# Performance work log

Measured on AMD Instinct MI355X. Metric: run time of the kernel, lower is better.

## Reference

```python
import math
import jax, jax.numpy as jnp
import numpy as np

B, T, F = 2, 1024, 1024
H, DK, DV = 16, 64, 64
OUT = 1024


def _rel_shift_left(x):
    # x: (b, h, t1, t2); Transformer-XL left shift + tril mask (causal part)
    b, h, t1, t2 = x.shape
    xp = jnp.pad(x, ((0, 0), (0, 0), (0, 0), (1, 0)))
    xp = xp.reshape(b, h, t2 + 1, t1)[:, :, 1:].reshape(b, h, t1, t2)
    tril = jnp.tril(jnp.ones((t1, t2), x.dtype), t2 - t1)
    return xp * tril


def _rel_shift_right(x):
    # x: (b, h, t1, t2); right shift + triu mask (non-causal part)
    b, h, t1, t2 = x.shape
    xp = jnp.pad(x, ((0, 0), (0, 0), (0, 0), (0, 1)))
    xp = xp.reshape(b, h, t2 + 1, t1)[:, :, :-1].reshape(b, h, t1, t2)
    triu = jnp.triu(jnp.ones((t1, t2), x.dtype), t2 - t1 + 1)
    return xp * triu


def setup_inputs() -> dict:
    key = jax.random.key(0)
    ks = jax.random.split(key, 16)
    s = 0.02
    return {
        'query': jax.random.normal(ks[0], (B, T, F), jnp.float32),
        'key': jax.random.normal(ks[1], (B, T, F), jnp.float32),
        'value': jax.random.normal(ks[2], (B, T, F), jnp.float32),
        'pos_emb': jax.random.normal(ks[3], (1, T, F), jnp.float32),
        'Wq': jax.random.normal(ks[4], (H * DK, F), jnp.float32) * s,
        'bq': jnp.zeros((H * DK,), jnp.float32),
        'Wk': jax.random.normal(ks[5], (H * DK, F), jnp.float32) * s,
        'bk': jnp.zeros((H * DK,), jnp.float32),
        'Wv': jax.random.normal(ks[6], (H * DV, F), jnp.float32) * s,
        'bv': jnp.zeros((H * DV,), jnp.float32),
        'Wp': jax.random.normal(ks[7], (H * DK, F), jnp.float32) * s,
        'bp': jnp.zeros((H * DK,), jnp.float32),
        'Wo': jax.random.normal(ks[8], (OUT, H * DV), jnp.float32) * s,
        'bo': jnp.zeros((OUT,), jnp.float32),
        'u_bias': jax.random.normal(ks[9], (H, DK), jnp.float32) * s,
        'v_bias': jax.random.normal(ks[10], (H, DK), jnp.float32) * s,
    }


def reference(query, key, value, pos_emb, Wq, bq, Wk, bk, Wv, bv, Wp, bp, Wo, bo, u_bias, v_bias):
    b, t1, _ = query.shape
    t2 = key.shape[1]
    q = (query @ Wq.T + bq).reshape(b, t1, H, DK)          # (b, t1, h, dk)
    k = (key @ Wk.T + bk).reshape(b, t2, H, DK).transpose(0, 2, 1, 3)   # (b, h, t2, dk)
    v = (value @ Wv.T + bv).reshape(b, t2, H, DV).transpose(0, 2, 1, 3) # (b, h, t2, dv)
    p = (pos_emb @ Wp.T + bp).reshape(pos_emb.shape[0], -1, H, DK).transpose(0, 2, 1, 3)[0]  # (h, t2, dk)

    q_plus_u = (q + u_bias).transpose(0, 2, 1, 3)  # (b, h, t1, dk)
    q_plus_v = (q + v_bias).transpose(0, 2, 1, 3)  # (b, h, t1, dk)

    AC = jnp.einsum('bhtd,bhsd->bhts', q_plus_u, k)
    BD = _rel_shift_left(jnp.einsum('bhtd,hsd->bhts', q_plus_v, p))
    # non-causal part: flip pos embeddings along time, right shift
    BD = BD + _rel_shift_right(jnp.einsum('bhtd,hsd->bhts', q_plus_v, jnp.flip(p, axis=1)))

    scores = (AC + BD) / math.sqrt(DK)
    attn = jax.nn.softmax(scores, axis=-1)
    x = jnp.einsum('bhts,bhsd->bthd', attn, v).reshape(b, t1, H * DV)
    return x @ Wo.T + bo
```

## Files before the change

kernel.cpp:

```cpp
#include <hip/hip_runtime.h>
#include <hip/hip_bf16.h>
#include <stdint.h>

typedef __attribute__((ext_vector_type(8))) short bf16x8;
typedef __attribute__((ext_vector_type(4))) float f32x4;
typedef __attribute__((ext_vector_type(4))) short short4v;
typedef __attribute__((ext_vector_type(2))) unsigned u32x2;

#define SCALE2 0.18033688011112042f

__device__ __forceinline__ short f2b(float f) {
  union { float f; unsigned u; } un; un.f = f;
  unsigned r = un.u + 0x7FFFu + ((un.u >> 16) & 1u);
  return (short)(r >> 16);
}

#define GLDS(GP, LP) __builtin_amdgcn_global_load_lds( \
    (__attribute__((address_space(1))) void*)(GP), \
    (__attribute__((address_space(3))) void*)(LP), 16, 0, 0)

struct CvtTab { const float* s[12]; short* d[12]; };

__global__ void cvt_all(CvtTab tab) {
  int chunk = blockIdx.x >> 10;
  int off = (blockIdx.x & 1023) * 256 + threadIdx.x;
  float4 v = *((const float4*)tab.s[chunk] + off);
  short4v o;
  o[0] = f2b(v.x); o[1] = f2b(v.y); o[2] = f2b(v.z); o[3] = f2b(v.w);
  *((short4v*)tab.d[chunk] + off) = o;
}

__device__ __forceinline__ void gemm_core128(
    const short* __restrict__ A, const short* __restrict__ W,
    int tile_m, int tile_n, short* lds, f32x4 acc[4][4])
{
  const int tid = threadIdx.x;
  const int wave = tid >> 6, lane = tid & 63;
  const int wr = wave >> 1, wc = wave & 1;
  const int q15 = lane & 15, q4 = lane >> 4;
  const int rl = lane >> 3;
  const int cswz = ((lane & 7) * 16) ^ (rl << 4);

#pragma unroll
  for (int i = 0; i < 4; ++i)
#pragma unroll
    for (int j = 0; j < 4; ++j) acc[i][j] = (f32x4){0.f, 0.f, 0.f, 0.f};

  auto stage = [&](int buf, int k0) {
    short* As = lds + buf * 16384;
    short* Bs = As + 8192;
#pragma unroll
    for (int s = 0; s < 4; ++s) {
      int ia = wave * 4 + s;
      int row = ia * 8 + rl;
      GLDS(A + (size_t)(tile_m + row) * 1024 + k0 + (cswz >> 1), (char*)As + ia * 1024);
      GLDS(W + (size_t)(tile_n + row) * 1024 + k0 + (cswz >> 1), (char*)Bs + ia * 1024);
    }
  };

  stage(0, 0);
  __syncthreads();
  for (int t = 0; t < 16; ++t) {
    const int cur = t & 1;
    if (t < 15) stage(cur ^ 1, (t + 1) * 64);
    const short* As = lds + cur * 16384;
    const short* Bs = As + 8192;
#pragma unroll
    for (int kk = 0; kk < 2; ++kk) {
      const int kbyte = kk * 64 + q4 * 16;
      const int rswz = (q15 & 7) << 4;
      bf16x8 af[4], bfr[4];
#pragma unroll
      for (int i = 0; i < 4; ++i)
        af[i] = *(const bf16x8*)((const char*)As + (wr * 64 + i * 16 + q15) * 128 + (kbyte ^ rswz));
#pragma unroll
      for (int j = 0; j < 4; ++j)
        bfr[j] = *(const bf16x8*)((const char*)Bs + (wc * 64 + j * 16 + q15) * 128 + (kbyte ^ rswz));
#pragma unroll
      for (int i = 0; i < 4; ++i)
#pragma unroll
        for (int j = 0; j < 4; ++j)
          acc[i][j] = __builtin_amdgcn_mfma_f32_16x16x32_bf16(af[i], bfr[j], acc[i][j], 0, 0, 0);
    }
    __syncthreads();
  }
}

__global__ __launch_bounds__(256)
void gemm_qkvp(const short* __restrict__ q_in, const short* __restrict__ k_in,
               const short* __restrict__ v_in, const short* __restrict__ p_in,
               const short* __restrict__ wq, const short* __restrict__ wk,
               const short* __restrict__ wv, const short* __restrict__ wp,
               const float* __restrict__ bq, const float* __restrict__ bk,
               const float* __restrict__ bv, const float* __restrict__ bp,
               const float* __restrict__ ub, const float* __restrict__ vb,
               short* __restrict__ qu, short* __restrict__ qv,
               short* __restrict__ kx, short* __restrict__ vtp, short* __restrict__ pp)
{
  __shared__ __align__(16) short lds[32768];
  const int n = blockIdx.x;
  const int by = n & 7;
  const int bx = n >> 3;
  const short* A; const short* W; const float* bias; int tm, mode;
  if (bx < 16)      { A = q_in; W = wq; bias = bq; tm = bx;      mode = 0; }
  else if (bx < 32) { A = k_in; W = wk; bias = bk; tm = bx - 16; mode = 1; }
  else if (bx < 48) { A = v_in; W = wv; bias = bv; tm = bx - 32; mode = 2; }
  else              { A = p_in; W = wp; bias = bp; tm = bx - 48; mode = 3; }

  f32x4 acc[4][4];
  gemm_core128(A, W, tm * 128, by * 128, lds, acc);

  const int lane = threadIdx.x & 63, wave = threadIdx.x >> 6;
  const int wr = wave >> 1, wc = wave & 1, q15 = lane & 15, q4 = lane >> 4;
#pragma unroll
  for (int i = 0; i < 4; ++i)
#pragma unroll
    for (int j = 0; j < 4; ++j)
#pragma unroll
      for (int r = 0; r < 4; ++r) {
        int m = tm * 128 + wr * 64 + i * 16 + q4 * 4 + r;
        int nn = by * 128 + wc * 64 + j * 16 + q15;
        float v = acc[i][j][r] + bias[nn];
        int bb = m >> 10, t = m & 1023, hh = nn >> 6, d = nn & 63;
        if (mode == 0) {
          size_t o = ((size_t)(bb * 16 + hh) * 1024 + t) * 64 + d;
          qu[o] = f2b((v + ub[nn]) * SCALE2);
          qv[o] = f2b((v + vb[nn]) * SCALE2);
        } else if (mode == 1) {
          kx[((size_t)(bb * 16 + hh) * 1024 + t) * 64 + d] = f2b(v);
        } else if (mode == 2) {
          vtp[((size_t)(bb * 16 + hh) * 64 + d) * 1024 + t] = f2b(v);
        } else {
          pp[((size_t)hh * 1024 + m) * 64 + d] = f2b(v);
        }
      }
}

__global__ __launch_bounds__(256)
void gemm_out(const short* __restrict__ X, const short* __restrict__ W,
              const float* __restrict__ bo, float* __restrict__ out)
{
  __shared__ __align__(16) short lds[24576];
  const int n = blockIdx.x;
  const int bxm = (n >> 3) & 15;
  const int byn = ((n & 7) << 1) | (n >> 7);
  const int tile_m = bxm * 128, tile_n = byn * 64;

  const int tid = threadIdx.x;
  const int wave = tid >> 6, lane = tid & 63;
  const int wr = wave >> 1, wc = wave & 1;
  const int q15 = lane & 15, q4 = lane >> 4;
  const int rl = lane >> 3;
  const int cswz = ((lane & 7) * 16) ^ (rl << 4);

  f32x4 acc[4][2];
#pragma unroll
  for (int i = 0; i < 4; ++i)
#pragma unroll
    for (int j = 0; j < 2; ++j) acc[i][j] = (f32x4){0.f, 0.f, 0.f, 0.f};

  auto stage = [&](int buf, int k0) {
    short* As = lds + buf * 12288;
    short* Bs = As + 8192;
#pragma unroll
    for (int s = 0; s < 6; ++s) {
      int idx = wave * 6 + s;
      if (idx < 16) {
        int row = idx * 8 + rl;
        GLDS(X + (size_t)(tile_m + row) * 1024 + k0 + (cswz >> 1), (char*)As + idx * 1024);
      } else {
        int i2 = idx - 16;
        int row = i2 * 8 + rl;
        GLDS(W + (size_t)(tile_n + row) * 1024 + k0 + (cswz >> 1), (char*)Bs + i2 * 1024);
      }
    }
  };

  stage(0, 0);
  __syncthreads();
  for (int t = 0; t < 16; ++t) {
    const int cur = t & 1;
    if (t < 15) stage(cur ^ 1, (t + 1) * 64);
    const short* As = lds + cur * 12288;
    const short* Bs = As + 8192;
#pragma unroll
    for (int kk = 0; kk < 2; ++kk) {
      const int kbyte = kk * 64 + q4 * 16;
      const int rswz = (q15 & 7) << 4;
      bf16x8 af[4], bfr[2];
#pragma unroll
      for (int i = 0; i < 4; ++i)
        af[i] = *(const bf16x8*)((const char*)As + (wr * 64 + i * 16 + q15) * 128 + (kbyte ^ rswz));
#pragma unroll
      for (int j = 0; j < 2; ++j)
        bfr[j] = *(const bf16x8*)((const char*)Bs + (wc * 32 + j * 16 + q15) * 128 + (kbyte ^ rswz));
#pragma unroll
      for (int i = 0; i < 4; ++i)
#pragma unroll
        for (int j = 0; j < 2; ++j)
          acc[i][j] = __builtin_amdgcn_mfma_f32_16x16x32_bf16(af[i], bfr[j], acc[i][j], 0, 0, 0);
    }
    __syncthreads();
  }

#pragma unroll
  for (int i = 0; i < 4; ++i)
#pragma unroll
    for (int j = 0; j < 2; ++j)
#pragma unroll
      for (int r = 0; r < 4; ++r) {
        int m = tile_m + wr * 64 + i * 16 + q4 * 4 + r;
        int nn = tile_n + wc * 32 + j * 16 + q15;
        out[(size_t)m * 1024 + nn] = acc[i][j][r] + bo[nn];
      }
}

__global__ __launch_bounds__(256, 4)
void attn_kernel(const short* __restrict__ qu, const short* __restrict__ qv,
                 const short* __restrict__ kmat, const short* __restrict__ vt,
                 const short* __restrict__ p,
                 float* __restrict__ Opart, float* __restrict__ larr)
{
  __shared__ __align__(16) short Ks[4096];
  __shared__ __align__(16) short Vs[4096];
  __shared__ __align__(16) short Bl[8192];
  __shared__ __align__(16) short Pl[4096];

  const int nB = blockIdx.x;
  const int o = (nB & 7) * 128 + (nB >> 3);
  const int t0 = (o & 15) * 64;
  const int h = (o >> 4) & 15;
  const int z = o >> 8;
  const int b = z >> 1, sh = z & 1;

  const int tid = threadIdx.x;
  const int wave = tid >> 6, lane = tid & 63;
  const int q15 = lane & 15, q4 = lane >> 4;
  const size_t bh = (size_t)(b * 16 + h);
  const short* pW = p + (size_t)h * 65536;
  const int rswz = (q15 & 7) << 4;
  char* BlW = (char*)Bl + wave * 4096;
  char* PlW = (char*)Pl + wave * 2048;
  const int blrow = q15 * 256;
  const int plrow = q15 * 128;

  const int srow = tid >> 3;
  const int scol = (tid & 7) * 8;
  const int sdst = srow * 128 + ((scol * 2) ^ ((srow & 7) << 4));

  const int sbeg = sh * 512, send = sbeg + 512;
  const short* kg = kmat + (bh * 1024 + sbeg + srow) * 64 + scol;
  const short* vg = vt + (bh * 64 + srow) * 1024 + sbeg + scol;

  bf16x8 quf[2], qvf[2];
  {
    size_t base = (bh * 1024 + t0 + wave * 16 + q15) * 64 + q4 * 8;
    quf[0] = *(const bf16x8*)(qu + base);
    quf[1] = *(const bf16x8*)(qu + base + 32);
    qvf[0] = *(const bf16x8*)(qv + base);
    qvf[1] = *(const bf16x8*)(qv + base + 32);
  }
  bf16x8 ones;
#pragma unroll
  for (int i = 0; i < 8; ++i) ones[i] = (short)0x3F80;

  f32x4 acco[4], accl;
#pragma unroll
  for (int g = 0; g < 4; ++g) acco[g] = (f32x4){0.f, 0.f, 0.f, 0.f};
  accl = (f32x4){0.f, 0.f, 0.f, 0.f};

  int live0 = -1, live1 = -1;

  auto refill = [&](int base) {
    f32x4 bacc[4];
#pragma unroll
    for (int g = 0; g < 4; ++g) bacc[g] = (f32x4){0.f, 0.f, 0.f, 0.f};
#pragma unroll
    for (int kc = 0; kc < 2; ++kc) {
      const int kof = kc * 32 + q4 * 8;
#pragma unroll
      for (int g = 0; g < 4; ++g) {
        bf16x8 pf = *(const bf16x8*)(pW + (size_t)(base + g * 16 + q15) * 64 + kof);
        bacc[g] = __builtin_amdgcn_mfma_f32_16x16x32_bf16(pf, qvf[kc], bacc[g], 0, 0, 0);
      }
    }
    const int pbase = base & 127;
#pragma unroll
    for (int g = 0; g < 4; ++g) {
      unsigned a0 = __float_as_uint(bacc[g][0]); a0 = a0 + 0x7FFFu + ((a0 >> 16) & 1u);
      unsigned a1 = __float_as_uint(bacc[g][1]); a1 = a1 + 0x7FFFu + ((a1 >> 16) & 1u);
      unsigned a2 = __float_as_uint(bacc[g][2]); a2 = a2 + 0x7FFFu + ((a2 >> 16) & 1u);
      unsigned a3 = __float_as_uint(bacc[g][3]); a3 = a3 + 0x7FFFu + ((a3 >> 16) & 1u);
      u32x2 pk;
      pk[0] = (a0 >> 16) | (a1 & 0xFFFF0000u);
      pk[1] = (a2 >> 16) | (a3 & 0xFFFF0000u);
      int inrow = (pbase + 16 * g + 4 * q4) * 2;
      *(u32x2*)(BlW + blrow + (inrow ^ rswz)) = pk;
    }
  };

  bf16x8 kr0 = *(const bf16x8*)kg;
  bf16x8 kr1 = *(const bf16x8*)(kg + 2048);
  bf16x8 vr0 = *(const bf16x8*)vg;
  bf16x8 vr1 = *(const bf16x8*)(vg + 32768);

  for (int s0 = sbeg; s0 < send; s0 += 64) {
    __syncthreads();
    *(bf16x8*)((char*)Ks + sdst) = kr0;
    *(bf16x8*)((char*)Ks + sdst + 4096) = kr1;
    *(bf16x8*)((char*)Vs + sdst) = vr0;
    *(bf16x8*)((char*)Vs + sdst + 4096) = vr1;
    __syncthreads();
    if (s0 + 64 < send) {
      kg += 4096; vg += 64;
      kr0 = *(const bf16x8*)kg;
      kr1 = *(const bf16x8*)(kg + 2048);
      vr0 = *(const bf16x8*)vg;
      vr1 = *(const bf16x8*)(vg + 32768);
    }

    f32x4 accac[4];
#pragma unroll
    for (int g = 0; g < 4; ++g) accac[g] = (f32x4){0.f, 0.f, 0.f, 0.f};
    __builtin_amdgcn_s_setprio(1);
#pragma unroll
    for (int kc = 0; kc < 2; ++kc) {
      const int kbyte = kc * 64 + q4 * 16;
#pragma unroll
      for (int g = 0; g < 4; ++g) {
        bf16x8 kf = *(const bf16x8*)((const char*)Ks + (g * 16 + q15) * 128 + (kbyte ^ rswz));
        accac[g] = __builtin_amdgcn_mfma_f32_16x16x32_bf16(kf, quf[kc], accac[g], 0, 0, 0);
      }
    }
    __builtin_amdgcn_s_setprio(0);

    const int dist0 = (t0 > s0) ? (t0 - s0) : (s0 - t0);
    const int jbase = 960 - dist0;
    {
      int sl = (jbase >> 6) & 1;
      bool nd = sl ? (live1 != jbase) : (live0 != jbase);
      if (nd) { refill(jbase); if (sl) live1 = jbase; else live0 = jbase; }
      int b1 = jbase + 64;
      if (b1 <= 960) {
        int sl1 = sl ^ 1;
        bool nd1 = sl1 ? (live1 != b1) : (live0 != b1);
        if (nd1) { refill(b1); if (sl1) live1 = b1; else live0 = b1; }
      }
    }
    const int JB = jbase & 127;

    unsigned pk01[4], pk23[4];
    if (s0 != t0) {
      const bool below = (s0 < t0);
#pragma unroll
      for (int g = 0; g < 4; ++g) {
        int K = below ? (63 - 16 * wave - q15 + 16 * g + 4 * q4)
                      : (60 + 16 * wave + q15 - 16 * g - 4 * q4);
        int lo = JB + K;
        int par = lo & 1;
        int C = lo & ~1;
        unsigned w0 = *(const unsigned*)(BlW + blrow + (((((C + 0) & 127) * 2)) ^ rswz));
        unsigned w1 = *(const unsigned*)(BlW + blrow + (((((C + 2) & 127) * 2)) ^ rswz));
        unsigned w2 = *(const unsigned*)(BlW + blrow + (((((C + 4) & 127) * 2)) ^ rswz));
        unsigned u0 = par ? ((w1 << 16) | (w0 >> 16)) : w0;
        unsigned u1 = par ? ((w2 << 16) | (w1 >> 16)) : w1;
        float bd0, bd1, bd2, bd3;
        if (below) {
          bd0 = __uint_as_float(u0 << 16); bd1 = __uint_as_float(u0 & 0xFFFF0000u);
          bd2 = __uint_as_float(u1 << 16); bd3 = __uint_as_float(u1 & 0xFFFF0000u);
        } else {
          bd3 = __uint_as_float(u0 << 16); bd2 = __uint_as_float(u0 & 0xFFFF0000u);
          bd1 = __uint_as_float(u1 << 16); bd0 = __uint_as_float(u1 & 0xFFFF0000u);
        }
        float e0 = __builtin_amdgcn_exp2f(accac[g][0] + bd0);
        float e1 = __builtin_amdgcn_exp2f(accac[g][1] + bd1);
        float e2 = __builtin_amdgcn_exp2f(accac[g][2] + bd2);
        float e3 = __builtin_amdgcn_exp2f(accac[g][3] + bd3);
        pk01[g] = (__float_as_uint(e0) >> 16) | (__float_as_uint(e1) & 0xFFFF0000u);
        pk23[g] = (__float_as_uint(e2) >> 16) | (__float_as_uint(e3) & 0xFFFF0000u);
      }
    } else {
      const int tl = 16 * wave + q15;
#pragma unroll
      for (int g = 0; g < 4; ++g) {
        float ev[4];
#pragma unroll
        for (int r = 0; r < 4; ++r) {
          int e = tl - (16 * g + 4 * q4 + r);
          int d = e < 0 ? -e : e;
          unsigned hv = *(const unsigned short*)(BlW + blrow + ((((127 - d) * 2)) ^ rswz));
          float bd = __uint_as_float(hv << 16);
          ev[r] = __builtin_amdgcn_exp2f(accac[g][r] + bd);
        }
        pk01[g] = (__float_as_uint(ev[0]) >> 16) | (__float_as_uint(ev[1]) & 0xFFFF0000u);
        pk23[g] = (__float_as_uint(ev[2]) >> 16) | (__float_as_uint(ev[3]) & 0xFFFF0000u);
      }
    }

#pragma unroll
    for (int g = 0; g < 4; ++g) {
      u32x2 pk; pk[0] = pk01[g]; pk[1] = pk23[g];
      int inrow = (16 * g + 4 * q4) * 2;
      *(u32x2*)(PlW + plrow + (inrow ^ rswz)) = pk;
    }

    __builtin_amdgcn_s_setprio(1);
#pragma unroll
    for (int kc = 0; kc < 2; ++kc) {
      const int kbyte = kc * 64 + q4 * 16;
      bf16x8 pf = *(const bf16x8*)(PlW + plrow + (kbyte ^ rswz));
      accl = __builtin_amdgcn_mfma_f32_16x16x32_bf16(ones, pf, accl, 0, 0, 0);
#pragma unroll
      for (int g = 0; g < 4; ++g) {
        bf16x8 vf = *(const bf16x8*)((const char*)Vs + (g * 16 + q15) * 128 + (kbyte ^ rswz));
        acco[g] = __builtin_amdgcn_mfma_f32_16x16x32_bf16(vf, pf, acco[g], 0, 0, 0);
      }
    }
    __builtin_amdgcn_s_setprio(0);
  }

  size_t obase = ((size_t)(sh * 2 + b) * 16 + h) * 1024;
  const int tt = t0 + wave * 16 + q15;
#pragma unroll
  for (int g = 0; g < 4; ++g)
    *(f32x4*)(Opart + (obase + tt) * 64 + 16 * g + 4 * q4) = acco[g];
  if (lane < 16) larr[obase + tt] = accl[0];
}

__global__ void combine_k(const float* __restrict__ O, const float* __restrict__ larr,
                          short* __restrict__ x)
{
  int i = blockIdx.x * 256 + threadIdx.x;
  int dv4 = i & 15, rest = i >> 4;
  float4 a0 = *(const float4*)(O + (size_t)rest * 64 + dv4 * 4);
  float4 a1 = *(const float4*)(O + 2097152 + (size_t)rest * 64 + dv4 * 4);
  float l0 = larr[rest], l1 = larr[32768 + rest];
  float inv = 1.0f / (l0 + l1);
  int bq = rest >> 14, hq = (rest >> 10) & 15, tq = rest & 1023;
  short4v o;
  o[0] = f2b((a0.x + a1.x) * inv);
  o[1] = f2b((a0.y + a1.y) * inv);
  o[2] = f2b((a0.z + a1.z) * inv);
  o[3] = f2b((a0.w + a1.w) * inv);
  *(short4v*)(x + ((size_t)(bq * 1024 + tq) * 1024 + hq * 64 + dv4 * 4)) = o;
}

extern "C" void kernel_launch(void* const* d_in, const int* in_sizes, int n_in,
                              void* d_out, int out_size, void* d_ws, size_t ws_size,
                              hipStream_t stream) {
  const float* query = (const float*)d_in[0];
  const float* key   = (const float*)d_in[1];
  const float* value = (const float*)d_in[2];
  const float* pos   = (const float*)d_in[3];
  const float* Wq = (const float*)d_in[4];  const float* bq = (const float*)d_in[5];
  const float* Wk = (const float*)d_in[6];  const float* bk = (const float*)d_in[7];
  const float* Wv = (const float*)d_in[8];  const float* bv = (const float*)d_in[9];
  const float* Wp = (const float*)d_in[10]; const float* bp = (const float*)d_in[11];
  const float* Wo = (const float*)d_in[12]; const float* bo = (const float*)d_in[13];
  const float* ub = (const float*)d_in[14]; const float* vb = (const float*)d_in[15];

  char* ws = (char*)d_ws;
  const size_t MB = 1 << 20;
  short* Wo_bf    = (short*)(ws);
  short* qu_bf    = (short*)(ws + 2 * MB);
  short* qv_bf    = (short*)(ws + 6 * MB);
  short* k_bf     = (short*)(ws + 10 * MB);
  short* vT_bf    = (short*)(ws + 14 * MB);
  short* p_bf     = (short*)(ws + 18 * MB);
  short* x_bf     = (short*)(ws + 20 * MB);
  short* query_bf = (short*)(ws + 24 * MB);
  short* key_bf   = (short*)(ws + 28 * MB);
  short* value_bf = (short*)(ws + 32 * MB);
  short* pos_bf   = (short*)(ws + 36 * MB);
  short* Wq_bf    = (short*)(ws + 38 * MB);
  short* Wk_bf    = (short*)(ws + 40 * MB);
  short* Wv_bf    = (short*)(ws + 42 * MB);
  short* Wp_bf    = (short*)(ws + 44 * MB);
  float* Opart = (float*)(ws + 24 * MB);
  float* larr  = (float*)(ws + 40 * MB);

  CvtTab tab;
  tab.s[0] = query;           tab.d[0] = query_bf;
  tab.s[1] = query + 1048576; tab.d[1] = query_bf + 1048576;
  tab.s[2] = key;             tab.d[2] = key_bf;
  tab.s[3] = key + 1048576;   tab.d[3] = key_bf + 1048576;
  tab.s[4] = value;           tab.d[4] = value_bf;
  tab.s[5] = value + 1048576; tab.d[5] = value_bf + 1048576;
  tab.s[6] = pos;             tab.d[6] = pos_bf;
  tab.s[7] = Wq;              tab.d[7] = Wq_bf;
  tab.s[8] = Wk;              tab.d[8] = Wk_bf;
  tab.s[9] = Wv;              tab.d[9] = Wv_bf;
  tab.s[10] = Wp;             tab.d[10] = Wp_bf;
  tab.s[11] = Wo;             tab.d[11] = Wo_bf;
  hipLaunchKernelGGL(cvt_all, dim3(12288), dim3(256), 0, stream, tab);

  hipLaunchKernelGGL(gemm_qkvp, dim3(448), dim3(256), 0, stream,
                     query_bf, key_bf, value_bf, pos_bf,
                     Wq_bf, Wk_bf, Wv_bf, Wp_bf,
                     bq, bk, bv, bp, ub, vb,
                     qu_bf, qv_bf, k_bf, vT_bf, p_bf);

  hipLaunchKernelGGL(attn_kernel, dim3(1024), dim3(256), 0, stream,
                     qu_bf, qv_bf, k_bf, vT_bf, p_bf, Opart, larr);

  hipLaunchKernelGGL(combine_k, dim3(2048), dim3(256), 0, stream,
                     Opart, larr, x_bf);

  hipLaunchKernelGGL(gemm_out, dim3(256), dim3(256), 0, stream,
                     x_bf, Wo_bf, bo, (float*)d_out);
}
```

Measured before the change: 116.7 us.

## Split attention into single-wave blocks reading K/V directly from global memory

The attention kernel moves from 256-thread blocks of four waves sharing K/V tiles staged in LDS to 64-thread single-wave blocks, each handling 16 query rows, with four times as many blocks. K and V fragments are loaded straight from global memory into registers, so there is no LDS staging and no __syncthreads. The relative-position window is recomputed per wave from the exact distance range. This removes barrier stalls and shrinks LDS use to raise occupancy, but gives up K/V reuse across waves, so each tile is fetched four times as often through the cache hierarchy.

```diff
diff --git a/kernel.cpp b/kernel.cpp
--- a/kernel.cpp
+++ b/kernel.cpp
@@ -215,46 +215,35 @@
       }
 }
 
-__global__ __launch_bounds__(256, 4)
+__global__ __launch_bounds__(64, 6)
 void attn_kernel(const short* __restrict__ qu, const short* __restrict__ qv,
                  const short* __restrict__ kmat, const short* __restrict__ vt,
                  const short* __restrict__ p,
                  float* __restrict__ Opart, float* __restrict__ larr)
 {
-  __shared__ __align__(16) short Ks[4096];
-  __shared__ __align__(16) short Vs[4096];
-  __shared__ __align__(16) short Bl[8192];
-  __shared__ __align__(16) short Pl[4096];
+  __shared__ __align__(16) short Bl[2048];
+  __shared__ __align__(16) short Pl[1024];
 
   const int nB = blockIdx.x;
-  const int o = (nB & 7) * 128 + (nB >> 3);
-  const int t0 = (o & 15) * 64;
-  const int h = (o >> 4) & 15;
-  const int z = o >> 8;
+  const int o = (nB & 7) * 512 + (nB >> 3);
+  const int tb = (o & 63) * 16;
+  const int h = (o >> 6) & 15;
+  const int z = o >> 10;
   const int b = z >> 1, sh = z & 1;
 
-  const int tid = threadIdx.x;
-  const int wave = tid >> 6, lane = tid & 63;
+  const int lane = threadIdx.x;
   const int q15 = lane & 15, q4 = lane >> 4;
   const size_t bh = (size_t)(b * 16 + h);
   const short* pW = p + (size_t)h * 65536;
+  const short* kB = kmat + bh * 65536;
+  const short* vB = vt + bh * 65536;
   const int rswz = (q15 & 7) << 4;
-  char* BlW = (char*)Bl + wave * 4096;
-  char* PlW = (char*)Pl + wave * 2048;
   const int blrow = q15 * 256;
   const int plrow = q15 * 128;
 
-  const int srow = tid >> 3;
-  const int scol = (tid & 7) * 8;
-  const int sdst = srow * 128 + ((scol * 2) ^ ((srow & 7) << 4));
-
-  const int sbeg = sh * 512, send = sbeg + 512;
-  const short* kg = kmat + (bh * 1024 + sbeg + srow) * 64 + scol;
-  const short* vg = vt + (bh * 64 + srow) * 1024 + sbeg + scol;
-
   bf16x8 quf[2], qvf[2];
   {
-    size_t base = (bh * 1024 + t0 + wave * 16 + q15) * 64 + q4 * 8;
+    size_t base = (bh * 1024 + tb + q15) * 64 + q4 * 8;
     quf[0] = *(const bf16x8*)(qu + base);
     quf[1] = *(const bf16x8*)(qu + base + 32);
     qvf[0] = *(const bf16x8*)(qv + base);
@@ -295,102 +284,94 @@
       pk[0] = (a0 >> 16) | (a1 & 0xFFFF0000u);
       pk[1] = (a2 >> 16) | (a3 & 0xFFFF0000u);
       int inrow = (pbase + 16 * g + 4 * q4) * 2;
-      *(u32x2*)(BlW + blrow + (inrow ^ rswz)) = pk;
+      *(u32x2*)((char*)Bl + blrow + (inrow ^ rswz)) = pk;
     }
   };
 
-  bf16x8 kr0 = *(const bf16x8*)kg;
-  bf16x8 kr1 = *(const bf16x8*)(kg + 2048);
-  bf16x8 vr0 = *(const bf16x8*)vg;
-  bf16x8 vr1 = *(const bf16x8*)(vg + 32768);
-
-  for (int s0 = sbeg; s0 < send; s0 += 64) {
-    __syncthreads();
-    *(bf16x8*)((char*)Ks + sdst) = kr0;
-    *(bf16x8*)((char*)Ks + sdst + 4096) = kr1;
-    *(bf16x8*)((char*)Vs + sdst) = vr0;
-    *(bf16x8*)((char*)Vs + sdst + 4096) = vr1;
-    __syncthreads();
-    if (s0 + 64 < send) {
-      kg += 4096; vg += 64;
-      kr0 = *(const bf16x8*)kg;
-      kr1 = *(const bf16x8*)(kg + 2048);
-      vr0 = *(const bf16x8*)vg;
-      vr1 = *(const bf16x8*)(vg + 32768);
+  auto ensure = [&](int base) {
+    if ((base >> 6) & 1) { if (live1 != base) { refill(base); live1 = base; } }
+    else                 { if (live0 != base) { refill(base); live0 = base; } }
+  };
+
+  const int sbeg = sh * 512;
+  for (int s0 = sbeg; s0 < sbeg + 512; s0 += 64) {
+    const int D = tb - s0;
+
+    {
+      int lo_ts = D - 63, hi_ts = D + 15;
+      int alo = lo_ts < 0 ? -lo_ts : lo_ts;
+      int ahi = hi_ts < 0 ? -hi_ts : hi_ts;
+      int amax = alo > ahi ? alo : ahi;
+      int amin = (lo_ts <= 0 && hi_ts >= 0) ? 0 : (alo < ahi ? alo : ahi);
+      int jmin = 1023 - amax, jmax = 1023 - amin;
+      int b0 = jmin & ~63;
+      ensure(b0);
+      if (jmax >= b0 + 64) ensure(b0 + 64);
     }
 
     f32x4 accac[4];
 #pragma unroll
     for (int g = 0; g < 4; ++g) accac[g] = (f32x4){0.f, 0.f, 0.f, 0.f};
-    __builtin_amdgcn_s_setprio(1);
 #pragma unroll
     for (int kc = 0; kc < 2; ++kc) {
-      const int kbyte = kc * 64 + q4 * 16;
+      const int kof = kc * 32 + q4 * 8;
+      bf16x8 kf[4];
+#pragma unroll
+      for (int g = 0; g < 4; ++g)
+        kf[g] = *(const bf16x8*)(kB + (s0 + 16 * g + q15) * 64 + kof);
+      __builtin_amdgcn_s_setprio(1);
+#pragma unroll
+      for (int g = 0; g < 4; ++g)
+        accac[g] = __builtin_amdgcn_mfma_f32_16x16x32_bf16(kf[g], quf[kc], accac[g], 0, 0, 0);
+      __builtin_amdgcn_s_setprio(0);
+    }
+
+    unsigned pk01[4], pk23[4];
+    if (D >= 64) {
 #pragma unroll
       for (int g = 0; g < 4; ++g) {
-        bf16x8 kf = *(const bf16x8*)((const char*)Ks + (g * 16 + q15) * 128 + (kbyte ^ rswz));
-        accac[g] = __builtin_amdgcn_mfma_f32_16x16x32_bf16(kf, quf[kc], accac[g], 0, 0, 0);
-      }
-    }
-    __builtin_amdgcn_s_setprio(0);
-
-    const int dist0 = (t0 > s0) ? (t0 - s0) : (s0 - t0);
-    const int jbase = 960 - dist0;
-    {
-      int sl = (jbase >> 6) & 1;
-      bool nd = sl ? (live1 != jbase) : (live0 != jbase);
-      if (nd) { refill(jbase); if (sl) live1 = jbase; else live0 = jbase; }
-      int b1 = jbase + 64;
-      if (b1 <= 960) {
-        int sl1 = sl ^ 1;
-        bool nd1 = sl1 ? (live1 != b1) : (live0 != b1);
-        if (nd1) { refill(b1); if (sl1) live1 = b1; else live0 = b1; }
-      }
-    }
-    const int JB = jbase & 127;
-
-    unsigned pk01[4], pk23[4];
-    if (s0 != t0) {
-      const bool below = (s0 < t0);
-#pragma unroll
-      for (int g = 0; g < 4; ++g) {
-        int K = below ? (63 - 16 * wave - q15 + 16 * g + 4 * q4)
-                      : (60 + 16 * wave + q15 - 16 * g - 4 * q4);
-        int lo = JB + K;
-        int par = lo & 1;
-        int C = lo & ~1;
-        unsigned w0 = *(const unsigned*)(BlW + blrow + (((((C + 0) & 127) * 2)) ^ rswz));
-        unsigned w1 = *(const unsigned*)(BlW + blrow + (((((C + 2) & 127) * 2)) ^ rswz));
-        unsigned w2 = *(const unsigned*)(BlW + blrow + (((((C + 4) & 127) * 2)) ^ rswz));
+        int lo = 1023 - D - q15 + 16 * g + 4 * q4;
+        int par = lo & 1, C = lo & ~1;
+        unsigned w0 = *(const unsigned*)((char*)Bl + blrow + ((((C + 0) & 127) * 2) ^ rswz));
+        unsigned w1 = *(const unsigned*)((char*)Bl + blrow + ((((C + 2) & 127) * 2) ^ rswz));
+        unsigned w2 = *(const unsigned*)((char*)Bl + blrow + ((((C + 4) & 127) * 2) ^ rswz));
         unsigned u0 = par ? ((w1 << 16) | (w0 >> 16)) : w0;
         unsigned u1 = par ? ((w2 << 16) | (w1 >> 16)) : w1;
-        float bd0, bd1, bd2, bd3;
-        if (below) {
-          bd0 = __uint_as_float(u0 << 16); bd1 = __uint_as_float(u0 & 0xFFFF0000u);
-          bd2 = __uint_as_float(u1 << 16); bd3 = __uint_as_float(u1 & 0xFFFF0000u);
-        } else {
-          bd3 = __uint_as_float(u0 << 16); bd2 = __uint_as_float(u0 & 0xFFFF0000u);
-          bd1 = __uint_as_float(u1 << 16); bd0 = __uint_as_float(u1 & 0xFFFF0000u);
-        }
-        float e0 = __builtin_amdgcn_exp2f(accac[g][0] + bd0);
-        float e1 = __builtin_amdgcn_exp2f(accac[g][1] + bd1);
-        float e2 = __builtin_amdgcn_exp2f(accac[g][2] + bd2);
-        float e3 = __builtin_amdgcn_exp2f(accac[g][3] + bd3);
+        float e0 = __builtin_amdgcn_exp2f(accac[g][0] + __uint_as_float(u0 << 16));
+        float e1 = __builtin_amdgcn_exp2f(accac[g][1] + __uint_as_float(u0 & 0xFFFF0000u));
+        float e2 = __builtin_amdgcn_exp2f(accac[g][2] + __uint_as_float(u1 << 16));
+        float e3 = __builtin_amdgcn_exp2f(accac[g][3] + __uint_as_float(u1 & 0xFFFF0000u));
         pk01[g] = (__float_as_uint(e0) >> 16) | (__float_as_uint(e1) & 0xFFFF0000u);
         pk23[g] = (__float_as_uint(e2) >> 16) | (__float_as_uint(e3) & 0xFFFF0000u);
       }
+    } else if (D <= -16) {
+#pragma unroll
+      for (int g = 0; g < 4; ++g) {
+        int lo = 1020 + D + q15 - 16 * g - 4 * q4;
+        int par = lo & 1, C = lo & ~1;
+        unsigned w0 = *(const unsigned*)((char*)Bl + blrow + ((((C + 0) & 127) * 2) ^ rswz));
+        unsigned w1 = *(const unsigned*)((char*)Bl + blrow + ((((C + 2) & 127) * 2) ^ rswz));
+        unsigned w2 = *(const unsigned*)((char*)Bl + blrow + ((((C + 4) & 127) * 2) ^ rswz));
+        unsigned u0 = par ? ((w1 << 16) | (w0 >> 16)) : w0;
+        unsigned u1 = par ? ((w2 << 16) | (w1 >> 16)) : w1;
+        float e3 = __builtin_amdgcn_exp2f(accac[g][3] + __uint_as_float(u0 << 16));
+        float e2 = __builtin_amdgcn_exp2f(accac[g][2] + __uint_as_float(u0 & 0xFFFF0000u));
+        float e1 = __builtin_amdgcn_exp2f(accac[g][1] + __uint_as_float(u1 << 16));
+        float e0 = __builtin_amdgcn_exp2f(accac[g][0] + __uint_as_float(u1 & 0xFFFF0000u));
+        pk01[g] = (__float_as_uint(e0) >> 16) | (__float_as_uint(e1) & 0xFFFF0000u);
+        pk23[g] = (__float_as_uint(e2) >> 16) | (__float_as_uint(e3) & 0xFFFF0000u);
+      }
     } else {
-      const int tl = 16 * wave + q15;
+      const int e0c = D + q15 - 4 * q4;
 #pragma unroll
       for (int g = 0; g < 4; ++g) {
         float ev[4];
 #pragma unroll
         for (int r = 0; r < 4; ++r) {
-          int e = tl - (16 * g + 4 * q4 + r);
+          int e = e0c - 16 * g - r;
           int d = e < 0 ? -e : e;
-          unsigned hv = *(const unsigned short*)(BlW + blrow + ((((127 - d) * 2)) ^ rswz));
-          float bd = __uint_as_float(hv << 16);
-          ev[r] = __builtin_amdgcn_exp2f(accac[g][r] + bd);
+          unsigned hv = *(const unsigned short*)((char*)Bl + blrow + ((((1023 - d) & 127) * 2) ^ rswz));
+          ev[r] = __builtin_amdgcn_exp2f(accac[g][r] + __uint_as_float(hv << 16));
         }
         pk01[g] = (__float_as_uint(ev[0]) >> 16) | (__float_as_uint(ev[1]) & 0xFFFF0000u);
         pk23[g] = (__float_as_uint(ev[2]) >> 16) | (__float_as_uint(ev[3]) & 0xFFFF0000u);
@@ -401,26 +382,29 @@
     for (int g = 0; g < 4; ++g) {
       u32x2 pk; pk[0] = pk01[g]; pk[1] = pk23[g];
       int inrow = (16 * g + 4 * q4) * 2;
-      *(u32x2*)(PlW + plrow + (inrow ^ rswz)) = pk;
-    }
-
-    __builtin_amdgcn_s_setprio(1);
+      *(u32x2*)((char*)Pl + plrow + (inrow ^ rswz)) = pk;
+    }
+
 #pragma unroll
     for (int kc = 0; kc < 2; ++kc) {
       const int kbyte = kc * 64 + q4 * 16;
-      bf16x8 pf = *(const bf16x8*)(PlW + plrow + (kbyte ^ rswz));
+      const int kof = kc * 32 + q4 * 8;
+      bf16x8 pf = *(const bf16x8*)((char*)Pl + plrow + (kbyte ^ rswz));
+      bf16x8 vf[4];
+#pragma unroll
+      for (int g = 0; g < 4; ++g)
+        vf[g] = *(const bf16x8*)(vB + (16 * g + q15) * 1024 + s0 + kof);
+      __builtin_amdgcn_s_setprio(1);
       accl = __builtin_amdgcn_mfma_f32_16x16x32_bf16(ones, pf, accl, 0, 0, 0);
 #pragma unroll
-      for (int g = 0; g < 4; ++g) {
-        bf16x8 vf = *(const bf16x8*)((const char*)Vs + (g * 16 + q15) * 128 + (kbyte ^ rswz));
-        acco[g] = __builtin_amdgcn_mfma_f32_16x16x32_bf16(vf, pf, acco[g], 0, 0, 0);
-      }
-    }
-    __builtin_amdgcn_s_setprio(0);
+      for (int g = 0; g < 4; ++g)
+        acco[g] = __builtin_amdgcn_mfma_f32_16x16x32_bf16(vf[g], pf, acco[g], 0, 0, 0);
+      __builtin_amdgcn_s_setprio(0);
+    }
   }
 
   size_t obase = ((size_t)(sh * 2 + b) * 16 + h) * 1024;
-  const int tt = t0 + wave * 16 + q15;
+  const int tt = tb + q15;
 #pragma unroll
   for (int g = 0; g < 4; ++g)
     *(f32x4*)(Opart + (obase + tt) * 64 + 16 * g + 4 * q4) = acco[g];
@@ -500,7 +484,7 @@
                      bq, bk, bv, bp, ub, vb,
                      qu_bf, qv_bf, k_bf, vT_bf, p_bf);
 
-  hipLaunchKernelGGL(attn_kernel, dim3(1024), dim3(256), 0, stream,
+  hipLaunchKernelGGL(attn_kernel, dim3(4096), dim3(64), 0, stream,
                      qu_bf, qv_bf, k_bf, vT_bf, p_bf, Opart, larr);
 
   hipLaunchKernelGGL(combine_k, dim3(2048), dim3(256), 0, stream,
```

Result: slower. 177.5 us (+52.1%).
